# Kernel tuning notes

Measured on AMD Instinct MI355X. Metric: run time of the kernel, lower is better.

## Reference

```python
import jax, jax.numpy as jnp
import numpy as np

B, C, H, W = 2, 4, 512, 512
V, F, A = 100000, 200000, 8


def setup_inputs() -> dict:
    key = jax.random.key(0)
    ks = jax.random.split(key, 10)
    vertex_pos = jax.random.normal(ks[0], (B, V, 3), dtype=jnp.float32)
    faces = jax.random.randint(ks[1], (F, 3), 0, V, dtype=jnp.int32)
    vert_adj_faces = jax.random.randint(ks[2], (V, A), 0, F, dtype=jnp.int32)
    w = jax.random.uniform(ks[3], (V, A), dtype=jnp.float32) + 1e-3
    vert_adj_weights = w / w.sum(-1, keepdims=True)
    intrinsics = jax.random.normal(ks[4], (B, C, 3, 3), dtype=jnp.float32)
    # make projective row well-conditioned: row 2 ~ [0,0,1]
    intrinsics = intrinsics.at[:, :, 2, :].set(jnp.array([0.0, 0.0, 1.0], jnp.float32))
    extrinsics = 0.1 * jax.random.normal(ks[5], (B, C, 3, 4), dtype=jnp.float32)
    extrinsics = extrinsics.at[:, :, 2, 3].add(5.0)  # keep camera-space z away from 0
    inverse_extrinsics = jax.random.normal(ks[6], (B, C, 4, 4), dtype=jnp.float32)
    inverse_extrinsics = inverse_extrinsics.at[:, :, 3, 3].set(1.0)
    fid = jax.random.randint(ks[7], (B, C, H, W), 0, F, dtype=jnp.int32)
    bg = jax.random.uniform(ks[8], (B, C, H, W)) < 0.5
    face_id = jnp.where(bg, -1, fid).astype(jnp.int32)
    bc = jax.random.uniform(ks[9], (B, C, H, W, 3), dtype=jnp.float32) + 1e-3
    barycentrics = bc / bc.sum(-1, keepdims=True)
    return {"vertex_pos": vertex_pos, "faces": faces, "vert_adj_faces": vert_adj_faces,
            "vert_adj_weights": vert_adj_weights, "intrinsics": intrinsics,
            "extrinsics": extrinsics, "inverse_extrinsics": inverse_extrinsics,
            "face_id": face_id, "barycentrics": barycentrics}


def _forward(vertex_pos, faces, vert_adj_faces, vert_adj_weights,
             intrinsics, extrinsics, inverse_extrinsics, face_id, barycentrics):
    # ---- face normals: gather face vertices, cross product ----
    fv = vertex_pos[:, faces]                                  # [B,F,3,3]
    face_normal = jnp.cross(fv[:, :, 1] - fv[:, :, 0], fv[:, :, 2] - fv[:, :, 0])  # [B,F,3]
    # ---- vertex normals: adjacency-weighted sum of face normals ----
    van = face_normal[:, vert_adj_faces]                       # [B,V,A,3]
    vertex_normal = jnp.einsum('bvac,va->bvc', van, vert_adj_weights)  # [B,V,3]
    # ---- projection: homogeneous verts through extrinsics then intrinsics ----
    homo = jnp.concatenate([vertex_pos, jnp.ones_like(vertex_pos[..., :1])], -1)  # [B,V,4]
    cv = jnp.einsum('bvk,bcjk->bcvj', homo, extrinsics)        # [B,C,V,3]
    iv = jnp.einsum('bcvk,bcjk->bcvj', cv, intrinsics)         # [B,C,V,3]
    iv = jnp.concatenate([iv[..., :2] / iv[..., 2:], iv[..., 2:]], -1)
    # ---- rasterized per-pixel gather + barycentric blend (masked, not scatter) ----
    mask = face_id >= 0                                        # [B,C,H,W]
    fid = jnp.where(mask, face_id, 0)
    vids = faces[fid]                                          # [B,C,H,W,3]
    gather_b = jax.vmap(lambda tab, idx: tab[idx])             # batched vertex gather
    pos_px = gather_b(vertex_pos, vids)                        # [B,C,H,W,3,3]
    nrm_px = gather_b(vertex_normal, vids)                     # [B,C,H,W,3,3]
    scr_px = jax.vmap(jax.vmap(lambda tab, idx: tab[idx]))(iv, vids)  # [B,C,H,W,3,3]
    bw = barycentrics[..., None]                               # [B,C,H,W,3,1]
    blended_pos = (pos_px * bw).sum(-2)                        # [B,C,H,W,3]
    blended_nrm = (nrm_px * bw).sum(-2)
    blended_scr = (scr_px * bw).sum(-2)
    nrm_unit = blended_nrm / jnp.clip(
        jnp.linalg.norm(blended_nrm, axis=-1, keepdims=True), 1e-12)  # F.normalize
    # ---- depth: distance from camera origin (from inverse extrinsics) ----
    cam_o = inverse_extrinsics[:, :, :, -1]
    cam_o = cam_o / cam_o[..., -1:]
    origin = cam_o[..., :3]                                    # [B,C,3]
    depth = jnp.linalg.norm(origin[:, :, None, None, :] - blended_pos,
                            axis=-1, keepdims=True)            # [B,C,H,W,1]
    m = mask[..., None]
    z3 = jnp.zeros_like(blended_pos)
    fg_img = jnp.broadcast_to(m, blended_pos.shape).astype(jnp.float32)
    pos_img = jnp.where(m, blended_pos, z3)
    nrm_img = jnp.where(m, nrm_unit, z3)
    dep_img = jnp.where(m, jnp.broadcast_to(depth, blended_pos.shape), z3)
    scr_img = jnp.where(m, blended_scr, z3)
    return jnp.stack([fg_img, pos_img, nrm_img, dep_img, scr_img], 0)  # [5,B,C,H,W,3]


def reference(vertex_pos, faces, vert_adj_faces, vert_adj_weights,
              intrinsics, extrinsics, inverse_extrinsics, face_id, barycentrics):
    return _forward(vertex_pos, faces, vert_adj_faces, vert_adj_weights,
                    intrinsics, extrinsics, inverse_extrinsics, face_id, barycentrics)
```

## Files before the change

kernel.cpp:

```cpp
#include <hip/hip_runtime.h>
#include <hip/hip_fp16.h>
#include <string.h>

#define B_ 2
#define C_ 4
#define H_ 512
#define W_ 512
#define V_ 100000
#define F_ 200000
#define A_ 8

#define HW_   (H_ * W_)
#define NPIX  (B_ * C_ * H_ * W_)
#define PLANE ((size_t)NPIX * 3)
#define PXB   512

typedef float f32x4 __attribute__((ext_vector_type(4)));

__device__ __forceinline__ float2 unpack2f(double d) {
    float2 t;
    memcpy(&t, &d, 8);
    return t;
}

__global__ void k_prep1(const float* __restrict__ vertex_pos,
                        const int* __restrict__ faces,
                        uint2* __restrict__ fn16,
                        unsigned long long* __restrict__ faces64) {
    int t = blockIdx.x * blockDim.x + threadIdx.x;
    if (t >= B_ * F_) return;
    int b = t / F_;
    int f = t - b * F_;
    int i0 = faces[f * 3 + 0];
    int i1 = faces[f * 3 + 1];
    int i2 = faces[f * 3 + 2];
    if (b == 0) {
        faces64[f] = (unsigned long long)(unsigned)i0 |
                     ((unsigned long long)(unsigned)i1 << 17) |
                     ((unsigned long long)(unsigned)i2 << 34);
    }
    const float* vp = vertex_pos + (size_t)b * V_ * 3;
    float p0x = vp[i0 * 3 + 0], p0y = vp[i0 * 3 + 1], p0z = vp[i0 * 3 + 2];
    float p1x = vp[i1 * 3 + 0], p1y = vp[i1 * 3 + 1], p1z = vp[i1 * 3 + 2];
    float p2x = vp[i2 * 3 + 0], p2y = vp[i2 * 3 + 1], p2z = vp[i2 * 3 + 2];
    float e1x = p1x - p0x, e1y = p1y - p0y, e1z = p1z - p0z;
    float e2x = p2x - p0x, e2y = p2y - p0y, e2z = p2z - p0z;
    float nx = e1y * e2z - e1z * e2y;
    float ny = e1z * e2x - e1x * e2z;
    float nz = e1x * e2y - e1y * e2x;
    __half2 h0 = __floats2half2_rn(nx, ny);
    __half2 h1 = __floats2half2_rn(nz, 0.f);
    fn16[t] = make_uint2(*reinterpret_cast<unsigned int*>(&h0),
                         *reinterpret_cast<unsigned int*>(&h1));
}

__global__ void k_prep2(const float* __restrict__ vertex_pos,
                        const float* __restrict__ intrinsics,
                        const float* __restrict__ extrinsics,
                        const uint2* __restrict__ fn16,
                        const int* __restrict__ vert_adj_faces,
                        const float* __restrict__ vert_adj_weights,
                        uint4* __restrict__ rec16) {
    int t = blockIdx.x * blockDim.x + threadIdx.x;
    if (t >= B_ * V_) return;
    int b = t / V_;
    int v = t - b * V_;

    const int* adj = vert_adj_faces + (size_t)v * A_;
    const float* wt = vert_adj_weights + (size_t)v * A_;
    const uint2* fn = fn16 + (size_t)b * F_;
    float ax = 0.f, ay = 0.f, az = 0.f;
#pragma unroll
    for (int a = 0; a < A_; ++a) {
        uint2 r = fn[adj[a]];
        float w = wt[a];
        float2 n01 = __half22float2(*reinterpret_cast<__half2*>(&r.x));
        float2 n2  = __half22float2(*reinterpret_cast<__half2*>(&r.y));
        ax += w * n01.x;
        ay += w * n01.y;
        az += w * n2.x;
    }
    const float* p = vertex_pos + (size_t)t * 3;
    float x = p[0], y = p[1], z = p[2];
    __half2 hxy = __floats2half2_rn(x, y);
    __half2 hzn = __floats2half2_rn(z, ax);
    __half2 hnn = __floats2half2_rn(ay, az);
    unsigned int w0 = *reinterpret_cast<unsigned int*>(&hxy);
    unsigned int w1 = *reinterpret_cast<unsigned int*>(&hzn);
    unsigned int w2 = *reinterpret_cast<unsigned int*>(&hnn);

#pragma unroll
    for (int c = 0; c < C_; ++c) {
        int bc = b * C_ + c;
        const float* E = extrinsics + (size_t)bc * 12;
        float cv0 = x * E[0] + y * E[1] + z * E[2]  + E[3];
        float cv1 = x * E[4] + y * E[5] + z * E[6]  + E[7];
        float cv2 = x * E[8] + y * E[9] + z * E[10] + E[11];
        const float* K = intrinsics + (size_t)bc * 9;
        float i0 = cv0 * K[0] + cv1 * K[1] + cv2 * K[2];
        float i1 = cv0 * K[3] + cv1 * K[4] + cv2 * K[5];
        float i2 = cv0 * K[6] + cv1 * K[7] + cv2 * K[8];
        __half2 hs = __floats2half2_rn(i0 / i2, i1 / i2);
        rec16[(size_t)bc * V_ + v] =
            make_uint4(w0, w1, w2, *reinterpret_cast<unsigned int*>(&hs));
    }
}

__global__ __launch_bounds__(256, 8) void k_pixel(
        const unsigned long long* __restrict__ faces64,
        const float* __restrict__ inverse_extrinsics,
        const float* __restrict__ extrinsics,
        const int* __restrict__ face_id,
        const float* __restrict__ bary,
        const uint4* __restrict__ rec16,
        float* __restrict__ out) {
    __shared__ float lds[PXB * 3];

    int nb = gridDim.x;
    int bid = blockIdx.x;
    int swz = (bid & 7) * (nb >> 3) + (bid >> 3);
    int tid = threadIdx.x;

    int base = swz * PXB + tid * 2;
    int bc = base >> 18;

    const float* ie = inverse_extrinsics + (size_t)bc * 16;
    float iw = ie[15];
    float ox = ie[3] / iw, oy = ie[7] / iw, oz = ie[11] / iw;
    const float* E = extrinsics + (size_t)bc * 12;
    float e8 = E[8], e9 = E[9], e10 = E[10], e11 = E[11];

    long long fid2 = __builtin_nontemporal_load((const long long*)(face_id + base));
    int fidv[2] = { (int)(fid2 & 0xFFFFFFFFll), (int)(fid2 >> 32) };

    const double* bp = (const double*)(bary + (size_t)base * 3);
    float2 q0 = unpack2f(__builtin_nontemporal_load(bp + 0));
    float2 q1 = unpack2f(__builtin_nontemporal_load(bp + 1));
    float2 q2 = unpack2f(__builtin_nontemporal_load(bp + 2));
    float bw[2][3] = {{q0.x, q0.y, q1.x}, {q1.y, q2.x, q2.y}};

    float fg[2], dep[2];
    float pos[2][3], nrm[2][3], sc[2][3];

#pragma unroll
    for (int k = 0; k < 2; ++k) {
        int fid = fidv[k];
        float w0 = bw[k][0], w1 = bw[k][1], w2 = bw[k][2];
        if (fid >= 0) {
            unsigned long long f3 = faces64[fid];
            int i0 = (int)(f3 & 0x1FFFF);
            int i1 = (int)((f3 >> 17) & 0x1FFFF);
            int i2 = (int)((f3 >> 34) & 0x1FFFF);

            size_t sbase = (size_t)bc * V_;
            uint4 A  = rec16[sbase + i0];
            uint4 Bv = rec16[sbase + i1];
            uint4 Cv = rec16[sbase + i2];

            float2 af0 = __half22float2(*reinterpret_cast<__half2*>(&A.x));
            float2 af1 = __half22float2(*reinterpret_cast<__half2*>(&A.y));
            float2 af2 = __half22float2(*reinterpret_cast<__half2*>(&A.z));
            float2 af3 = __half22float2(*reinterpret_cast<__half2*>(&A.w));
            float2 bf0 = __half22float2(*reinterpret_cast<__half2*>(&Bv.x));
            float2 bf1 = __half22float2(*reinterpret_cast<__half2*>(&Bv.y));
            float2 bf2 = __half22float2(*reinterpret_cast<__half2*>(&Bv.z));
            float2 bf3 = __half22float2(*reinterpret_cast<__half2*>(&Bv.w));
            float2 cf0 = __half22float2(*reinterpret_cast<__half2*>(&Cv.x));
            float2 cf1 = __half22float2(*reinterpret_cast<__half2*>(&Cv.y));
            float2 cf2 = __half22float2(*reinterpret_cast<__half2*>(&Cv.z));
            float2 cf3 = __half22float2(*reinterpret_cast<__half2*>(&Cv.w));

            float px = w0 * af0.x + w1 * bf0.x + w2 * cf0.x;
            float py = w0 * af0.y + w1 * bf0.y + w2 * cf0.y;
            float pz = w0 * af1.x + w1 * bf1.x + w2 * cf1.x;
            float nx = w0 * af1.y + w1 * bf1.y + w2 * cf1.y;
            float ny = w0 * af2.x + w1 * bf2.x + w2 * cf2.x;
            float nz = w0 * af2.y + w1 * bf2.y + w2 * cf2.y;
            float sx = w0 * af3.x + w1 * bf3.x + w2 * cf3.x;
            float sy = w0 * af3.y + w1 * bf3.y + w2 * cf3.y;
            float sz = e8 * px + e9 * py + e10 * pz + e11;

            float nlen = fmaxf(sqrtf(nx * nx + ny * ny + nz * nz), 1e-12f);
            nx /= nlen; ny /= nlen; nz /= nlen;

            float dx = ox - px, dy = oy - py, dz = oz - pz;
            fg[k] = 1.f;
            dep[k] = sqrtf(dx * dx + dy * dy + dz * dz);
            pos[k][0] = px; pos[k][1] = py; pos[k][2] = pz;
            nrm[k][0] = nx; nrm[k][1] = ny; nrm[k][2] = nz;
            sc[k][0] = sx; sc[k][1] = sy; sc[k][2] = sz;
        } else {
            fg[k] = 0.f; dep[k] = 0.f;
            pos[k][0] = pos[k][1] = pos[k][2] = 0.f;
            nrm[k][0] = nrm[k][1] = nrm[k][2] = 0.f;
            sc[k][0] = sc[k][1] = sc[k][2] = 0.f;
        }
    }

    const int CHUNKS = PXB * 3 / 4;
    size_t blockbase = (size_t)swz * (PXB * 3);
    float* Lt = &lds[tid * 6];

#define EMIT_PLANE(P, V0, V1, V2, V3, V4, V5)                                   \
    {                                                                           \
        Lt[0] = (V0); Lt[1] = (V1); Lt[2] = (V2);                               \
        Lt[3] = (V3); Lt[4] = (V4); Lt[5] = (V5);                               \
        __syncthreads();                                                        \
        float* dst = out + (size_t)(P) * PLANE + blockbase;                     \
        for (int j = tid; j < CHUNKS; j += 256) {                               \
            f32x4 v = *(const f32x4*)&lds[j * 4];                               \
            __builtin_nontemporal_store(v, (f32x4*)dst + j);                    \
        }                                                                       \
        __syncthreads();                                                        \
    }

    EMIT_PLANE(0, fg[0], fg[0], fg[0], fg[1], fg[1], fg[1])
    EMIT_PLANE(1, pos[0][0], pos[0][1], pos[0][2], pos[1][0], pos[1][1], pos[1][2])
    EMIT_PLANE(2, nrm[0][0], nrm[0][1], nrm[0][2], nrm[1][0], nrm[1][1], nrm[1][2])
    EMIT_PLANE(3, dep[0], dep[0], dep[0], dep[1], dep[1], dep[1])
    EMIT_PLANE(4, sc[0][0], sc[0][1], sc[0][2], sc[1][0], sc[1][1], sc[1][2])
#undef EMIT_PLANE
}

extern "C" void kernel_launch(void* const* d_in, const int* in_sizes, int n_in,
                              void* d_out, int out_size, void* d_ws, size_t ws_size,
                              hipStream_t stream) {
    const float* vertex_pos         = (const float*)d_in[0];
    const int*   faces              = (const int*)  d_in[1];
    const int*   vert_adj_faces     = (const int*)  d_in[2];
    const float* vert_adj_weights   = (const float*)d_in[3];
    const float* intrinsics         = (const float*)d_in[4];
    const float* extrinsics         = (const float*)d_in[5];
    const float* inverse_extrinsics = (const float*)d_in[6];
    const int*   face_id            = (const int*)  d_in[7];
    const float* barycentrics       = (const float*)d_in[8];
    float* out = (float*)d_out;
    char* ws = (char*)d_ws;
    const int TPB = 256;

    uint2*              fn16    = (uint2*)             (ws + 0);
    unsigned long long* faces64 = (unsigned long long*)(ws + 3200000);
    uint4*              rec16   = (uint4*)             (ws + 4800000);

    hipLaunchKernelGGL(k_prep1, dim3((B_ * F_ + TPB - 1) / TPB), dim3(TPB), 0, stream,
                       vertex_pos, faces, fn16, faces64);
    hipLaunchKernelGGL(k_prep2, dim3((B_ * V_ + TPB - 1) / TPB), dim3(TPB), 0, stream,
                       vertex_pos, intrinsics, extrinsics, fn16,
                       vert_adj_faces, vert_adj_weights, rec16);
    hipLaunchKernelGGL(k_pixel, dim3(NPIX / PXB), dim3(TPB), 0, stream,
                       faces64, inverse_extrinsics, extrinsics, face_id, barycentrics,
                       rec16, out);
}
```

Measured before the change: 80.54 us.

## Hoist gathers branch-free with masking and double-buffer LDS output staging

Background pixels now clamp their face id to 0 and still run the full gather and compute, with results multiplied by a 0/1 mask. This lets all six rec16 gathers and both face loads be issued up front for more memory-level parallelism. The LDS staging buffer is doubled so each plane needs only one barrier instead of two. In exchange, background pixels (about half) now do gathers they previously skipped, which adds memory traffic, and LDS use per block doubles, which may lower occupancy.

```diff
diff --git a/kernel.cpp b/kernel.cpp
--- a/kernel.cpp
+++ b/kernel.cpp
@@ -114,7 +114,7 @@
         const float* __restrict__ bary,
         const uint4* __restrict__ rec16,
         float* __restrict__ out) {
-    __shared__ float lds[PXB * 3];
+    __shared__ float lds[2][PXB * 3];
 
     int nb = gridDim.x;
     int bid = blockIdx.x;
@@ -131,95 +131,113 @@
     float e8 = E[8], e9 = E[9], e10 = E[10], e11 = E[11];
 
     long long fid2 = __builtin_nontemporal_load((const long long*)(face_id + base));
-    int fidv[2] = { (int)(fid2 & 0xFFFFFFFFll), (int)(fid2 >> 32) };
+    int f0 = (int)(fid2 & 0xFFFFFFFFll);
+    int f1 = (int)(fid2 >> 32);
+    float sel0 = (f0 >= 0) ? 1.f : 0.f;
+    float sel1 = (f1 >= 0) ? 1.f : 0.f;
+    int c0 = (f0 >= 0) ? f0 : 0;
+    int c1 = (f1 >= 0) ? f1 : 0;
+
+    unsigned long long F0 = faces64[c0];
+    unsigned long long F1 = faces64[c1];
 
     const double* bp = (const double*)(bary + (size_t)base * 3);
     float2 q0 = unpack2f(__builtin_nontemporal_load(bp + 0));
     float2 q1 = unpack2f(__builtin_nontemporal_load(bp + 1));
     float2 q2 = unpack2f(__builtin_nontemporal_load(bp + 2));
+
+    size_t sbase = (size_t)bc * V_;
+    uint4 A0 = rec16[sbase + (int)(F0 & 0x1FFFF)];
+    uint4 B0 = rec16[sbase + (int)((F0 >> 17) & 0x1FFFF)];
+    uint4 C0 = rec16[sbase + (int)((F0 >> 34) & 0x1FFFF)];
+    uint4 A1 = rec16[sbase + (int)(F1 & 0x1FFFF)];
+    uint4 B1 = rec16[sbase + (int)((F1 >> 17) & 0x1FFFF)];
+    uint4 C1 = rec16[sbase + (int)((F1 >> 34) & 0x1FFFF)];
+
     float bw[2][3] = {{q0.x, q0.y, q1.x}, {q1.y, q2.x, q2.y}};
+    float selv[2] = {sel0, sel1};
+    const uint4* R[2][3] = {{&A0, &B0, &C0}, {&A1, &B1, &C1}};
 
     float fg[2], dep[2];
     float pos[2][3], nrm[2][3], sc[2][3];
 
 #pragma unroll
     for (int k = 0; k < 2; ++k) {
-        int fid = fidv[k];
         float w0 = bw[k][0], w1 = bw[k][1], w2 = bw[k][2];
-        if (fid >= 0) {
-            unsigned long long f3 = faces64[fid];
-            int i0 = (int)(f3 & 0x1FFFF);
-            int i1 = (int)((f3 >> 17) & 0x1FFFF);
-            int i2 = (int)((f3 >> 34) & 0x1FFFF);
-
-            size_t sbase = (size_t)bc * V_;
-            uint4 A  = rec16[sbase + i0];
-            uint4 Bv = rec16[sbase + i1];
-            uint4 Cv = rec16[sbase + i2];
-
-            float2 af0 = __half22float2(*reinterpret_cast<__half2*>(&A.x));
-            float2 af1 = __half22float2(*reinterpret_cast<__half2*>(&A.y));
-            float2 af2 = __half22float2(*reinterpret_cast<__half2*>(&A.z));
-            float2 af3 = __half22float2(*reinterpret_cast<__half2*>(&A.w));
-            float2 bf0 = __half22float2(*reinterpret_cast<__half2*>(&Bv.x));
-            float2 bf1 = __half22float2(*reinterpret_cast<__half2*>(&Bv.y));
-            float2 bf2 = __half22float2(*reinterpret_cast<__half2*>(&Bv.z));
-            float2 bf3 = __half22float2(*reinterpret_cast<__half2*>(&Bv.w));
-            float2 cf0 = __half22float2(*reinterpret_cast<__half2*>(&Cv.x));
-            float2 cf1 = __half22float2(*reinterpret_cast<__half2*>(&Cv.y));
-            float2 cf2 = __half22float2(*reinterpret_cast<__half2*>(&Cv.z));
-            float2 cf3 = __half22float2(*reinterpret_cast<__half2*>(&Cv.w));
-
-            float px = w0 * af0.x + w1 * bf0.x + w2 * cf0.x;
-            float py = w0 * af0.y + w1 * bf0.y + w2 * cf0.y;
-            float pz = w0 * af1.x + w1 * bf1.x + w2 * cf1.x;
-            float nx = w0 * af1.y + w1 * bf1.y + w2 * cf1.y;
-            float ny = w0 * af2.x + w1 * bf2.x + w2 * cf2.x;
-            float nz = w0 * af2.y + w1 * bf2.y + w2 * cf2.y;
-            float sx = w0 * af3.x + w1 * bf3.x + w2 * cf3.x;
-            float sy = w0 * af3.y + w1 * bf3.y + w2 * cf3.y;
-            float sz = e8 * px + e9 * py + e10 * pz + e11;
-
-            float nlen = fmaxf(sqrtf(nx * nx + ny * ny + nz * nz), 1e-12f);
-            nx /= nlen; ny /= nlen; nz /= nlen;
-
-            float dx = ox - px, dy = oy - py, dz = oz - pz;
-            fg[k] = 1.f;
-            dep[k] = sqrtf(dx * dx + dy * dy + dz * dz);
-            pos[k][0] = px; pos[k][1] = py; pos[k][2] = pz;
-            nrm[k][0] = nx; nrm[k][1] = ny; nrm[k][2] = nz;
-            sc[k][0] = sx; sc[k][1] = sy; sc[k][2] = sz;
-        } else {
-            fg[k] = 0.f; dep[k] = 0.f;
-            pos[k][0] = pos[k][1] = pos[k][2] = 0.f;
-            nrm[k][0] = nrm[k][1] = nrm[k][2] = 0.f;
-            sc[k][0] = sc[k][1] = sc[k][2] = 0.f;
-        }
+        uint4 A = *R[k][0], Bv = *R[k][1], Cv = *R[k][2];
+
+        float2 af0 = __half22float2(*reinterpret_cast<__half2*>(&A.x));
+        float2 af1 = __half22float2(*reinterpret_cast<__half2*>(&A.y));
+        float2 af2 = __half22float2(*reinterpret_cast<__half2*>(&A.z));
+        float2 af3 = __half22float2(*reinterpret_cast<__half2*>(&A.w));
+        float2 bf0 = __half22float2(*reinterpret_cast<__half2*>(&Bv.x));
+        float2 bf1 = __half22float2(*reinterpret_cast<__half2*>(&Bv.y));
+        float2 bf2 = __half22float2(*reinterpret_cast<__half2*>(&Bv.z));
+        float2 bf3 = __half22float2(*reinterpret_cast<__half2*>(&Bv.w));
+        float2 cf0 = __half22float2(*reinterpret_cast<__half2*>(&Cv.x));
+        float2 cf1 = __half22float2(*reinterpret_cast<__half2*>(&Cv.y));
+        float2 cf2 = __half22float2(*reinterpret_cast<__half2*>(&Cv.z));
+        float2 cf3 = __half22float2(*reinterpret_cast<__half2*>(&Cv.w));
+
+        float px = w0 * af0.x + w1 * bf0.x + w2 * cf0.x;
+        float py = w0 * af0.y + w1 * bf0.y + w2 * cf0.y;
+        float pz = w0 * af1.x + w1 * bf1.x + w2 * cf1.x;
+        float nx = w0 * af1.y + w1 * bf1.y + w2 * cf1.y;
+        float ny = w0 * af2.x + w1 * bf2.x + w2 * cf2.x;
+        float nz = w0 * af2.y + w1 * bf2.y + w2 * cf2.y;
+        float sx = w0 * af3.x + w1 * bf3.x + w2 * cf3.x;
+        float sy = w0 * af3.y + w1 * bf3.y + w2 * cf3.y;
+        float sz = e8 * px + e9 * py + e10 * pz + e11;
+
+        float nlen = fmaxf(sqrtf(nx * nx + ny * ny + nz * nz), 1e-12f);
+        nx /= nlen; ny /= nlen; nz /= nlen;
+
+        float dx = ox - px, dy = oy - py, dz = oz - pz;
+        float dd = sqrtf(dx * dx + dy * dy + dz * dz);
+
+        float s = selv[k];
+        fg[k] = s;
+        dep[k] = s * dd;
+        pos[k][0] = s * px; pos[k][1] = s * py; pos[k][2] = s * pz;
+        nrm[k][0] = s * nx; nrm[k][1] = s * ny; nrm[k][2] = s * nz;
+        sc[k][0] = s * sx; sc[k][1] = s * sy; sc[k][2] = s * sz;
     }
 
     const int CHUNKS = PXB * 3 / 4;
     size_t blockbase = (size_t)swz * (PXB * 3);
-    float* Lt = &lds[tid * 6];
-
-#define EMIT_PLANE(P, V0, V1, V2, V3, V4, V5)                                   \
+
+#define STAGE(BUF, V0, V1, V2, V3, V4, V5)                                      \
     {                                                                           \
+        float* Lt = &lds[BUF][tid * 6];                                         \
         Lt[0] = (V0); Lt[1] = (V1); Lt[2] = (V2);                               \
         Lt[3] = (V3); Lt[4] = (V4); Lt[5] = (V5);                               \
-        __syncthreads();                                                        \
+    }
+#define STORE(BUF, P)                                                           \
+    {                                                                           \
         float* dst = out + (size_t)(P) * PLANE + blockbase;                     \
         for (int j = tid; j < CHUNKS; j += 256) {                               \
-            f32x4 v = *(const f32x4*)&lds[j * 4];                               \
+            f32x4 v = *(const f32x4*)&lds[BUF][j * 4];                          \
             __builtin_nontemporal_store(v, (f32x4*)dst + j);                    \
         }                                                                       \
-        __syncthreads();                                                        \
-    }
-
-    EMIT_PLANE(0, fg[0], fg[0], fg[0], fg[1], fg[1], fg[1])
-    EMIT_PLANE(1, pos[0][0], pos[0][1], pos[0][2], pos[1][0], pos[1][1], pos[1][2])
-    EMIT_PLANE(2, nrm[0][0], nrm[0][1], nrm[0][2], nrm[1][0], nrm[1][1], nrm[1][2])
-    EMIT_PLANE(3, dep[0], dep[0], dep[0], dep[1], dep[1], dep[1])
-    EMIT_PLANE(4, sc[0][0], sc[0][1], sc[0][2], sc[1][0], sc[1][1], sc[1][2])
-#undef EMIT_PLANE
+    }
+
+    STAGE(0, fg[0], fg[0], fg[0], fg[1], fg[1], fg[1])
+    __syncthreads();
+    STORE(0, 0)
+    STAGE(1, pos[0][0], pos[0][1], pos[0][2], pos[1][0], pos[1][1], pos[1][2])
+    __syncthreads();
+    STORE(1, 1)
+    STAGE(0, nrm[0][0], nrm[0][1], nrm[0][2], nrm[1][0], nrm[1][1], nrm[1][2])
+    __syncthreads();
+    STORE(0, 2)
+    STAGE(1, dep[0], dep[0], dep[0], dep[1], dep[1], dep[1])
+    __syncthreads();
+    STORE(1, 3)
+    STAGE(0, sc[0][0], sc[0][1], sc[0][2], sc[1][0], sc[1][1], sc[1][2])
+    __syncthreads();
+    STORE(0, 4)
+#undef STAGE
+#undef STORE
 }
 
 extern "C" void kernel_launch(void* const* d_in, const int* in_sizes, int n_in,
```

New measurement: 89.00 us. 10.5% more time.
